# Optimization experiments

Measured on AMD Instinct MI355X. Metric: run time of the kernel, lower is better.

The kernel has to match this reference:

```python
import jax, jax.numpy as jnp
import numpy as np
from jax import lax

N_NODES = 10000
N_EDGES = 320000


def setup_inputs() -> dict:
    key = jax.random.key(0)
    ks = jax.random.split(key, 7)
    B, H, N, F = 4, 24, N_NODES, 32
    hid = 64
    x = jax.random.normal(ks[0], (B, H, N, F), dtype=jnp.float32)
    mask = jax.random.uniform(ks[1], (B, H), dtype=jnp.float32)
    edge_index = jax.random.randint(ks[2], (2, N_EDGES), 0, N, dtype=jnp.int32)
    W1 = jax.random.normal(ks[3], (F + 1, hid), dtype=jnp.float32) * (1.0 / np.sqrt(F + 1))
    b1 = jax.random.normal(ks[4], (hid,), dtype=jnp.float32) * 0.02
    W2 = jax.random.normal(ks[5], (hid, F), dtype=jnp.float32) * (1.0 / np.sqrt(hid))
    b2 = jax.random.normal(ks[6], (F,), dtype=jnp.float32) * 0.02
    return {"x": x, "mask": mask, "edge_index": edge_index,
            "W1": W1, "b1": b1, "W2": W2, "b2": b2}


def _gcn_norm(edge_index, num_nodes):
    # PyG GCNConv default: add self loops, symmetric normalization.
    loops = jnp.arange(num_nodes, dtype=edge_index.dtype)
    src = jnp.concatenate([edge_index[0], loops])
    dst = jnp.concatenate([edge_index[1], loops])
    deg = jax.ops.segment_sum(jnp.ones_like(dst, dtype=jnp.float32), dst,
                              num_segments=num_nodes)
    dinv = jnp.where(deg > 0, lax.rsqrt(jnp.maximum(deg, 1e-12)), 0.0)
    norm = dinv[src] * dinv[dst]  # [E']
    return src, dst, norm


def reference(x, mask, edge_index, W1, b1, W2, b2):
    B, H, N, F = x.shape
    src, dst, norm = _gcn_norm(edge_index, N)

    def gcn(h, W, b):
        # h: [B, N, Fin] -> lin, then normalized neighbor aggregation, then bias
        hw = h @ W                                   # [B, N, Fout]
        msg = hw[:, src, :].transpose(1, 0, 2)       # [E', B, Fout]
        msg = msg * norm[:, None, None]
        agg = jax.ops.segment_sum(msg, dst, num_segments=N)  # [N, B, Fout]
        return agg.transpose(1, 0, 2) + b

    def per_hour(carry, inp):
        xh, mh = inp                                 # xh: [B, N, F], mh: [B]
        mc = jnp.broadcast_to(mh[:, None, None], (B, N, 1))
        h = jnp.concatenate([xh, mc], axis=-1)       # [B, N, F+1]
        out = jnp.tanh(gcn(gcn(h, W1, b1), W2, b2))  # [B, N, F]
        return carry, out

    _, outs = lax.scan(per_hour, None,
                       (x.transpose(1, 0, 2, 3), mask.T))  # [H, B, N, F]
    return outs.transpose(1, 0, 2, 3)                     # [B, H, N, F]
```

## Files before the change

kernel.cpp:

```cpp
#include <hip/hip_runtime.h>
#include <hip/hip_fp16.h>

#define NN 10000
#define FF 32
#define PG 4
#define NGRP 24

__device__ __forceinline__ unsigned short f2h(float f){
  union { unsigned short s; _Float16 h; } c; c.h = (_Float16)f; return c.s;
}

__device__ __forceinline__ void fmix2(float& ax, float& ay, float w, unsigned h){
  asm("v_fma_mix_f32 %0, %2, %3, %0 op_sel_hi:[0,1,0]\n\t"
      "v_fma_mix_f32 %1, %2, %3, %1 op_sel:[0,1,0] op_sel_hi:[0,1,0]"
      : "+v"(ax), "+v"(ay) : "v"(w), "v"(h));
}

__global__ void k_count(const int* __restrict__ dst, int* __restrict__ cnt, int E){
  int e = blockIdx.x * 256 + threadIdx.x;
  if (e < E) atomicAdd(&cnt[dst[e]], 1);
}

__global__ __launch_bounds__(1024) void k_scan(const int* __restrict__ cnt,
                                               int* __restrict__ off,
                                               float* __restrict__ dinv,
                                               const float* __restrict__ W1,
                                               const float* __restrict__ W2,
                                               const float* __restrict__ b1,
                                               float* __restrict__ W12,
                                               float* __restrict__ bb){
  __shared__ int wsum[16];
  __shared__ int carry;
  int tid = threadIdx.x, lane = tid & 63, wv = tid >> 6;
  if (tid == 0) carry = 0;
  __syncthreads();
  for (int base = 0; base < NN; base += 1024){
    int i = base + tid;
    int c = (i < NN) ? cnt[i] : 0;
    int v = (c + 3) & ~3;
    int s = v;
    #pragma unroll
    for (int o = 1; o < 64; o <<= 1){
      int t = __shfl_up(s, o, 64);
      if (lane >= o) s += t;
    }
    if (lane == 63) wsum[wv] = s;
    __syncthreads();
    if (tid == 0){
      int a = carry;
      #pragma unroll
      for (int k = 0; k < 16; ++k){ int t = wsum[k]; wsum[k] = a; a += t; }
      carry = a;
    }
    __syncthreads();
    if (i < NN){
      off[i]  = wsum[wv] + s - v;
      dinv[i] = rsqrtf((float)(c + 1));
    }
    __syncthreads();
  }
  if (tid == 0) off[NN] = carry;
  for (int idx = tid; idx < 33 * 32; idx += 1024){
    int k = idx >> 5, j = idx & 31;
    float s = 0.f;
    for (int m = 0; m < 64; ++m) s += W1[k * 64 + m] * W2[m * 32 + j];
    W12[idx] = s;
  }
  if (tid < 32){
    int j = tid;
    float s = 0.f;
    for (int m = 0; m < 64; ++m) s += b1[m] * W2[m * 32 + j];
    bb[j] = s;
  }
}

__global__ void k_scatter(const int* __restrict__ ei, const int* __restrict__ off,
                          int* __restrict__ cur, const float* __restrict__ dinv,
                          int2* __restrict__ csr, int E){
  int e = blockIdx.x * 256 + threadIdx.x;
  if (e >= E) return;
  int s = ei[e], d = ei[E + e];
  int pos = off[d] + atomicAdd(&cur[d], 1);
  csr[pos] = make_int2(s << 8, __float_as_int(dinv[s]));
}

__global__ void k_srow(const int* __restrict__ off, const int2* __restrict__ csr,
                       const float* __restrict__ dinv, float* __restrict__ srow){
  int n = blockIdx.x * 256 + threadIdx.x;
  if (n >= NN) return;
  float a = dinv[n];
  int e0 = off[n], e1 = off[n + 1];
  for (int j = e0; j < e1; ++j) a += __int_as_float(csr[j].y);
  srow[n] = dinv[n] * a;
}

__global__ __launch_bounds__(256) void k_gemm1(const float* __restrict__ x,
    const float* __restrict__ mask, const float* __restrict__ W12,
    unsigned* __restrict__ hw){
  const int pg = blockIdx.y;
  const int n  = blockIdx.x * 256 + threadIdx.x;
  const int grp = pg >> 2, p = pg & 3;
  const float mv = mask[pg];
  float acc[32];
  #pragma unroll
  for (int f = 0; f < 32; ++f) acc[f] = mv * W12[32 * 32 + f];
  if (n >= NN) return;
  const float4* xp = (const float4*)(x + (size_t)pg * (NN * FF) + (size_t)n * FF);
  float xv[32];
  #pragma unroll
  for (int i = 0; i < 8; ++i){
    float4 v = xp[i];
    xv[4*i]   = v.x; xv[4*i+1] = v.y;
    xv[4*i+2] = v.z; xv[4*i+3] = v.w;
  }
  #pragma unroll
  for (int k = 0; k < 32; ++k){
    const float xk = xv[k];
    #pragma unroll
    for (int f = 0; f < 32; ++f) acc[f] += xk * W12[k * 32 + f];
  }
  unsigned* hwg = hw + (size_t)grp * (NN * 64) + ((size_t)n << 6) + (p << 4);
  #pragma unroll
  for (int j = 0; j < 4; ++j){
    uint4 u;
    u.x = (unsigned)f2h(acc[8*j+0]) | ((unsigned)f2h(acc[8*j+1]) << 16);
    u.y = (unsigned)f2h(acc[8*j+2]) | ((unsigned)f2h(acc[8*j+3]) << 16);
    u.z = (unsigned)f2h(acc[8*j+4]) | ((unsigned)f2h(acc[8*j+5]) << 16);
    u.w = (unsigned)f2h(acc[8*j+6]) | ((unsigned)f2h(acc[8*j+7]) << 16);
    ((uint4*)hwg)[j] = u;
  }
}

__device__ __forceinline__ void map_block(int bx, int& grp, int& chunk){
  int r  = bx / 5000;
  int w8 = bx % 5000;
  grp   = r * 8 + (w8 & 7);
  chunk = w8 >> 3;
}

__device__ __forceinline__ void agg_edges(int e0, int e1,
    const int2* __restrict__ csr, const char* __restrict__ Vb, int loff,
    float& ax, float& ay){
  int nq = (e1 - e0) >> 2;
  if (nq <= 0) return;
  const int4* c4 = (const int4*)(csr + e0);
  int qlast = nq - 1;
  int4 ca0 = c4[0], cb0 = c4[1];
  int i1 = (1 <= qlast) ? 1 : qlast;
  int4 ca1 = c4[2 * i1], cb1 = c4[2 * i1 + 1];
  unsigned r0 = *(const unsigned*)(Vb + (unsigned)(ca0.x + loff));
  unsigned r1 = *(const unsigned*)(Vb + (unsigned)(ca0.z + loff));
  unsigned r2 = *(const unsigned*)(Vb + (unsigned)(cb0.x + loff));
  unsigned r3 = *(const unsigned*)(Vb + (unsigned)(cb0.z + loff));
  for (int q = 0; q < nq; ++q){
    unsigned s0 = *(const unsigned*)(Vb + (unsigned)(ca1.x + loff));
    unsigned s1 = *(const unsigned*)(Vb + (unsigned)(ca1.z + loff));
    unsigned s2 = *(const unsigned*)(Vb + (unsigned)(cb1.x + loff));
    unsigned s3 = *(const unsigned*)(Vb + (unsigned)(cb1.z + loff));
    int i2 = (q + 2 <= qlast) ? q + 2 : qlast;
    int4 na = c4[2 * i2], nb = c4[2 * i2 + 1];
    fmix2(ax, ay, __int_as_float(ca0.y), r0);
    fmix2(ax, ay, __int_as_float(ca0.w), r1);
    fmix2(ax, ay, __int_as_float(cb0.y), r2);
    fmix2(ax, ay, __int_as_float(cb0.w), r3);
    ca0 = ca1; cb0 = cb1; ca1 = na; cb1 = nb;
    r0 = s0; r1 = s1; r2 = s2; r3 = s3;
  }
}

__global__ __launch_bounds__(256) void k_agg1(const int* __restrict__ off,
    const int2* __restrict__ csr, const float* __restrict__ dinv,
    const unsigned int* __restrict__ V, unsigned int* __restrict__ T){
  int grp, chunk; map_block(blockIdx.x, grp, chunk);
  int tid = threadIdx.x;
  int l = tid & 63;
  int wv = __builtin_amdgcn_readfirstlane(tid) >> 6;
  const char* Vb = (const char*)(V + (size_t)grp * (NN * 64));
  unsigned int* Tg = T + (size_t)grp * (NN * 64);
  int loff = l * 4;
  for (int it = 0; it < 4; ++it){
    int n = chunk * 16 + wv * 4 + it;
    float din = dinv[n];
    int e0 = off[n], e1 = off[n + 1];
    unsigned sv = *(const unsigned*)(Vb + (unsigned)((n << 8) + loff));
    float ax = 0.f, ay = 0.f;
    fmix2(ax, ay, din, sv);
    agg_edges(e0, e1, csr, Vb, loff, ax, ay);
    Tg[((size_t)n << 6) + l] =
        (unsigned)f2h(din * ax) | ((unsigned)f2h(din * ay) << 16);
  }
}

__global__ __launch_bounds__(256) void k_agg2(const int* __restrict__ off,
    const int2* __restrict__ csr, const float* __restrict__ dinv,
    const float* __restrict__ srow, const float* __restrict__ bb,
    const float* __restrict__ b2, const unsigned int* __restrict__ V,
    float* __restrict__ out){
  int grp, chunk; map_block(blockIdx.x, grp, chunk);
  int tid = threadIdx.x;
  int l = tid & 63;
  int wv = __builtin_amdgcn_readfirstlane(tid) >> 6;
  int p = l >> 4, fi = l & 15;
  const char* Vb = (const char*)(V + (size_t)grp * (NN * 64));
  int pg = grp * PG + p;
  float2 bbq = ((const float2*)bb)[fi];
  float2 b2q = ((const float2*)b2)[fi];
  float* outp = out + (size_t)pg * (NN * FF);
  int loff = l * 4;
  for (int it = 0; it < 4; ++it){
    int n = chunk * 16 + wv * 4 + it;
    float din = dinv[n];
    int e0 = off[n], e1 = off[n + 1];
    unsigned sv = *(const unsigned*)(Vb + (unsigned)((n << 8) + loff));
    float ax = 0.f, ay = 0.f;
    fmix2(ax, ay, din, sv);
    agg_edges(e0, e1, csr, Vb, loff, ax, ay);
    float sr = srow[n];
    float2 o;
    o.x = tanhf(din * ax + sr * bbq.x + b2q.x);
    o.y = tanhf(din * ay + sr * bbq.y + b2q.y);
    ((float2*)(outp + (size_t)n * FF))[fi] = o;
  }
}

extern "C" void kernel_launch(void* const* d_in, const int* in_sizes, int n_in,
                              void* d_out, int out_size, void* d_ws, size_t ws_size,
                              hipStream_t stream){
  const float* x    = (const float*)d_in[0];
  const float* mask = (const float*)d_in[1];
  const int*   ei   = (const int*)d_in[2];
  const float* W1   = (const float*)d_in[3];
  const float* b1   = (const float*)d_in[4];
  const float* W2   = (const float*)d_in[5];
  const float* b2   = (const float*)d_in[6];
  float* out = (float*)d_out;
  const int E = in_sizes[2] / 2;
  const int CSRCAP = E + 3 * NN + 64;

  char* wsp = (char*)d_ws;
  auto alloc = [&](size_t bytes) -> char* {
    char* p = wsp; wsp += (bytes + 255) & ~(size_t)255; return p;
  };
  int*   cnt  = (int*)  alloc((size_t)NN * 4);
  int*   off  = (int*)  alloc((size_t)(NN + 1) * 4);
  int*   cur  = (int*)  alloc((size_t)NN * 4);
  float* dinv = (float*)alloc((size_t)NN * 4);
  float* srow = (float*)alloc((size_t)NN * 4);
  float* W12  = (float*)alloc(33 * 32 * 4);
  float* bbv  = (float*)alloc(32 * 4);
  int2*  csr  = (int2*) alloc((size_t)CSRCAP * 8);
  const size_t per_group = (size_t)NN * 64 * 4;
  unsigned int* hw = (unsigned int*)alloc((size_t)NGRP * per_group);
  unsigned int* t1 = (unsigned int*)alloc((size_t)NGRP * per_group);

  hipMemsetAsync(cnt, 0, (size_t)NN * 4, stream);
  hipMemsetAsync(cur, 0, (size_t)NN * 4, stream);
  hipMemsetAsync(csr, 0, (size_t)CSRCAP * 8, stream);
  k_count  <<<(E + 255) / 256, 256, 0, stream>>>(ei + E, cnt, E);
  k_scan   <<<1, 1024, 0, stream>>>(cnt, off, dinv, W1, W2, b1, W12, bbv);
  k_scatter<<<(E + 255) / 256, 256, 0, stream>>>(ei, off, cur, dinv, csr, E);
  k_srow   <<<(NN + 255) / 256, 256, 0, stream>>>(off, csr, dinv, srow);

  k_gemm1<<<dim3(40, 96), 256, 0, stream>>>(x, mask, W12, hw);
  k_agg1 <<<15000, 256, 0, stream>>>(off, csr, dinv, hw, t1);
  k_agg2 <<<15000, 256, 0, stream>>>(off, csr, dinv, srow, bbv, b2, t1, out);
}
```

Before: 557.0 us.

## Aggregate three feature groups per block to reuse CSR edge loads

Each aggregation block now processes three groups (t3, t3+8, t3+16) for the same node chunk, so CSR indices and weights are loaded once and reused for three gathers. The grid shrinks from 15000 to 5000 blocks. This cuts redundant CSR traffic and index arithmetic and adds memory-level parallelism per thread. In exchange it raises register pressure and lowers block count, which may hurt occupancy.

```diff
diff --git a/kernel.cpp b/kernel.cpp
--- a/kernel.cpp
+++ b/kernel.cpp
@@ -131,16 +131,11 @@
   }
 }
 
-__device__ __forceinline__ void map_block(int bx, int& grp, int& chunk){
-  int r  = bx / 5000;
-  int w8 = bx % 5000;
-  grp   = r * 8 + (w8 & 7);
-  chunk = w8 >> 3;
-}
-
-__device__ __forceinline__ void agg_edges(int e0, int e1,
-    const int2* __restrict__ csr, const char* __restrict__ Vb, int loff,
-    float& ax, float& ay){
+__device__ __forceinline__ void agg_edges3(int e0, int e1,
+    const int2* __restrict__ csr,
+    const char* __restrict__ V0, const char* __restrict__ V1,
+    const char* __restrict__ V2, int loff,
+    float& ax0, float& ay0, float& ax1, float& ay1, float& ax2, float& ay2){
   int nq = (e1 - e0) >> 2;
   if (nq <= 0) return;
   const int4* c4 = (const int4*)(csr + e0);
@@ -148,46 +143,68 @@
   int4 ca0 = c4[0], cb0 = c4[1];
   int i1 = (1 <= qlast) ? 1 : qlast;
   int4 ca1 = c4[2 * i1], cb1 = c4[2 * i1 + 1];
-  unsigned r0 = *(const unsigned*)(Vb + (unsigned)(ca0.x + loff));
-  unsigned r1 = *(const unsigned*)(Vb + (unsigned)(ca0.z + loff));
-  unsigned r2 = *(const unsigned*)(Vb + (unsigned)(cb0.x + loff));
-  unsigned r3 = *(const unsigned*)(Vb + (unsigned)(cb0.z + loff));
+  unsigned a0 = (unsigned)(ca0.x + loff), a1 = (unsigned)(ca0.z + loff);
+  unsigned a2 = (unsigned)(cb0.x + loff), a3 = (unsigned)(cb0.z + loff);
+  unsigned r00 = *(const unsigned*)(V0 + a0), r01 = *(const unsigned*)(V0 + a1);
+  unsigned r02 = *(const unsigned*)(V0 + a2), r03 = *(const unsigned*)(V0 + a3);
+  unsigned r10 = *(const unsigned*)(V1 + a0), r11 = *(const unsigned*)(V1 + a1);
+  unsigned r12 = *(const unsigned*)(V1 + a2), r13 = *(const unsigned*)(V1 + a3);
+  unsigned r20 = *(const unsigned*)(V2 + a0), r21 = *(const unsigned*)(V2 + a1);
+  unsigned r22 = *(const unsigned*)(V2 + a2), r23 = *(const unsigned*)(V2 + a3);
   for (int q = 0; q < nq; ++q){
-    unsigned s0 = *(const unsigned*)(Vb + (unsigned)(ca1.x + loff));
-    unsigned s1 = *(const unsigned*)(Vb + (unsigned)(ca1.z + loff));
-    unsigned s2 = *(const unsigned*)(Vb + (unsigned)(cb1.x + loff));
-    unsigned s3 = *(const unsigned*)(Vb + (unsigned)(cb1.z + loff));
+    unsigned b0 = (unsigned)(ca1.x + loff), b1 = (unsigned)(ca1.z + loff);
+    unsigned b2 = (unsigned)(cb1.x + loff), b3 = (unsigned)(cb1.z + loff);
+    unsigned s00 = *(const unsigned*)(V0 + b0), s01 = *(const unsigned*)(V0 + b1);
+    unsigned s02 = *(const unsigned*)(V0 + b2), s03 = *(const unsigned*)(V0 + b3);
+    unsigned s10 = *(const unsigned*)(V1 + b0), s11 = *(const unsigned*)(V1 + b1);
+    unsigned s12 = *(const unsigned*)(V1 + b2), s13 = *(const unsigned*)(V1 + b3);
+    unsigned s20 = *(const unsigned*)(V2 + b0), s21 = *(const unsigned*)(V2 + b1);
+    unsigned s22 = *(const unsigned*)(V2 + b2), s23 = *(const unsigned*)(V2 + b3);
     int i2 = (q + 2 <= qlast) ? q + 2 : qlast;
     int4 na = c4[2 * i2], nb = c4[2 * i2 + 1];
-    fmix2(ax, ay, __int_as_float(ca0.y), r0);
-    fmix2(ax, ay, __int_as_float(ca0.w), r1);
-    fmix2(ax, ay, __int_as_float(cb0.y), r2);
-    fmix2(ax, ay, __int_as_float(cb0.w), r3);
+    float w0 = __int_as_float(ca0.y), w1 = __int_as_float(ca0.w);
+    float w2 = __int_as_float(cb0.y), w3 = __int_as_float(cb0.w);
+    fmix2(ax0, ay0, w0, r00); fmix2(ax0, ay0, w1, r01);
+    fmix2(ax0, ay0, w2, r02); fmix2(ax0, ay0, w3, r03);
+    fmix2(ax1, ay1, w0, r10); fmix2(ax1, ay1, w1, r11);
+    fmix2(ax1, ay1, w2, r12); fmix2(ax1, ay1, w3, r13);
+    fmix2(ax2, ay2, w0, r20); fmix2(ax2, ay2, w1, r21);
+    fmix2(ax2, ay2, w2, r22); fmix2(ax2, ay2, w3, r23);
     ca0 = ca1; cb0 = cb1; ca1 = na; cb1 = nb;
-    r0 = s0; r1 = s1; r2 = s2; r3 = s3;
+    r00 = s00; r01 = s01; r02 = s02; r03 = s03;
+    r10 = s10; r11 = s11; r12 = s12; r13 = s13;
+    r20 = s20; r21 = s21; r22 = s22; r23 = s23;
   }
 }
 
 __global__ __launch_bounds__(256) void k_agg1(const int* __restrict__ off,
     const int2* __restrict__ csr, const float* __restrict__ dinv,
     const unsigned int* __restrict__ V, unsigned int* __restrict__ T){
-  int grp, chunk; map_block(blockIdx.x, grp, chunk);
+  int t3 = blockIdx.x & 7, chunk = blockIdx.x >> 3;
   int tid = threadIdx.x;
   int l = tid & 63;
   int wv = __builtin_amdgcn_readfirstlane(tid) >> 6;
-  const char* Vb = (const char*)(V + (size_t)grp * (NN * 64));
-  unsigned int* Tg = T + (size_t)grp * (NN * 64);
+  const char* V0 = (const char*)(V + (size_t)(t3     ) * (NN * 64));
+  const char* V1 = (const char*)(V + (size_t)(t3 +  8) * (NN * 64));
+  const char* V2 = (const char*)(V + (size_t)(t3 + 16) * (NN * 64));
+  unsigned int* T0 = T + (size_t)(t3     ) * (NN * 64);
+  unsigned int* T1 = T + (size_t)(t3 +  8) * (NN * 64);
+  unsigned int* T2 = T + (size_t)(t3 + 16) * (NN * 64);
   int loff = l * 4;
   for (int it = 0; it < 4; ++it){
     int n = chunk * 16 + wv * 4 + it;
     float din = dinv[n];
     int e0 = off[n], e1 = off[n + 1];
-    unsigned sv = *(const unsigned*)(Vb + (unsigned)((n << 8) + loff));
-    float ax = 0.f, ay = 0.f;
-    fmix2(ax, ay, din, sv);
-    agg_edges(e0, e1, csr, Vb, loff, ax, ay);
-    Tg[((size_t)n << 6) + l] =
-        (unsigned)f2h(din * ax) | ((unsigned)f2h(din * ay) << 16);
+    unsigned so = (unsigned)((n << 8) + loff);
+    float ax0 = 0.f, ay0 = 0.f, ax1 = 0.f, ay1 = 0.f, ax2 = 0.f, ay2 = 0.f;
+    fmix2(ax0, ay0, din, *(const unsigned*)(V0 + so));
+    fmix2(ax1, ay1, din, *(const unsigned*)(V1 + so));
+    fmix2(ax2, ay2, din, *(const unsigned*)(V2 + so));
+    agg_edges3(e0, e1, csr, V0, V1, V2, loff, ax0, ay0, ax1, ay1, ax2, ay2);
+    size_t ti = ((size_t)n << 6) + l;
+    T0[ti] = (unsigned)f2h(din * ax0) | ((unsigned)f2h(din * ay0) << 16);
+    T1[ti] = (unsigned)f2h(din * ax1) | ((unsigned)f2h(din * ay1) << 16);
+    T2[ti] = (unsigned)f2h(din * ax2) | ((unsigned)f2h(din * ay2) << 16);
   }
 }
 
@@ -196,30 +213,40 @@
     const float* __restrict__ srow, const float* __restrict__ bb,
     const float* __restrict__ b2, const unsigned int* __restrict__ V,
     float* __restrict__ out){
-  int grp, chunk; map_block(blockIdx.x, grp, chunk);
+  int t3 = blockIdx.x & 7, chunk = blockIdx.x >> 3;
   int tid = threadIdx.x;
   int l = tid & 63;
   int wv = __builtin_amdgcn_readfirstlane(tid) >> 6;
   int p = l >> 4, fi = l & 15;
-  const char* Vb = (const char*)(V + (size_t)grp * (NN * 64));
-  int pg = grp * PG + p;
+  const char* V0 = (const char*)(V + (size_t)(t3     ) * (NN * 64));
+  const char* V1 = (const char*)(V + (size_t)(t3 +  8) * (NN * 64));
+  const char* V2 = (const char*)(V + (size_t)(t3 + 16) * (NN * 64));
   float2 bbq = ((const float2*)bb)[fi];
   float2 b2q = ((const float2*)b2)[fi];
-  float* outp = out + (size_t)pg * (NN * FF);
+  float* out0 = out + (size_t)((t3     ) * PG + p) * (NN * FF);
+  float* out1 = out + (size_t)((t3 +  8) * PG + p) * (NN * FF);
+  float* out2 = out + (size_t)((t3 + 16) * PG + p) * (NN * FF);
   int loff = l * 4;
   for (int it = 0; it < 4; ++it){
     int n = chunk * 16 + wv * 4 + it;
     float din = dinv[n];
     int e0 = off[n], e1 = off[n + 1];
-    unsigned sv = *(const unsigned*)(Vb + (unsigned)((n << 8) + loff));
-    float ax = 0.f, ay = 0.f;
-    fmix2(ax, ay, din, sv);
-    agg_edges(e0, e1, csr, Vb, loff, ax, ay);
+    unsigned so = (unsigned)((n << 8) + loff);
+    float ax0 = 0.f, ay0 = 0.f, ax1 = 0.f, ay1 = 0.f, ax2 = 0.f, ay2 = 0.f;
+    fmix2(ax0, ay0, din, *(const unsigned*)(V0 + so));
+    fmix2(ax1, ay1, din, *(const unsigned*)(V1 + so));
+    fmix2(ax2, ay2, din, *(const unsigned*)(V2 + so));
+    agg_edges3(e0, e1, csr, V0, V1, V2, loff, ax0, ay0, ax1, ay1, ax2, ay2);
     float sr = srow[n];
-    float2 o;
-    o.x = tanhf(din * ax + sr * bbq.x + b2q.x);
-    o.y = tanhf(din * ay + sr * bbq.y + b2q.y);
-    ((float2*)(outp + (size_t)n * FF))[fi] = o;
+    float bx_ = sr * bbq.x + b2q.x, by_ = sr * bbq.y + b2q.y;
+    float2 o0, o1, o2;
+    o0.x = tanhf(din * ax0 + bx_); o0.y = tanhf(din * ay0 + by_);
+    o1.x = tanhf(din * ax1 + bx_); o1.y = tanhf(din * ay1 + by_);
+    o2.x = tanhf(din * ax2 + bx_); o2.y = tanhf(din * ay2 + by_);
+    size_t ni = (size_t)n * FF;
+    ((float2*)(out0 + ni))[fi] = o0;
+    ((float2*)(out1 + ni))[fi] = o1;
+    ((float2*)(out2 + ni))[fi] = o2;
   }
 }
 
@@ -262,6 +289,6 @@
   k_srow   <<<(NN + 255) / 256, 256, 0, stream>>>(off, csr, dinv, srow);
 
   k_gemm1<<<dim3(40, 96), 256, 0, stream>>>(x, mask, W12, hw);
-  k_agg1 <<<15000, 256, 0, stream>>>(off, csr, dinv, hw, t1);
-  k_agg2 <<<15000, 256, 0, stream>>>(off, csr, dinv, srow, bbv, b2, t1, out);
-}
+  k_agg1 <<<5000, 256, 0, stream>>>(off, csr, dinv, hw, t1);
+  k_agg2 <<<5000, 256, 0, stream>>>(off, csr, dinv, srow, bbv, b2, t1, out);
+}
```

Measured after the change: 642.6 us. 1.15x slower.
